# Performance work log

Measured on AMD Instinct MI355X. Metric: run time of the kernel, lower is better.

The kernel has to match this reference:

```python
import jax, jax.numpy as jnp
import numpy as np

FACTOR = 5


def setup_inputs() -> dict:
    key = jax.random.key(0)
    k1, k2, k3 = jax.random.split(key, 3)
    B, L, H, E = 8, 3072, 8, 64
    return {
        "queries": jax.random.normal(k1, (B, L, H, E), dtype=jnp.float32),
        "keys": jax.random.normal(k2, (B, L, H, E), dtype=jnp.float32),
        "values": jax.random.normal(k3, (B, L, H, E), dtype=jnp.float32),
        "attn_mask": jnp.zeros((1,), dtype=jnp.int32),  # unused, matches torch signature
    }


def _autocorrelation(queries, keys, values):
    B, L, H, E = queries.shape
    # L == S here, so keys/values are used as-is (torch path: values[:, :L])
    qp = jnp.transpose(queries, (0, 2, 3, 1))  # [B,H,E,L]
    kp = jnp.transpose(keys, (0, 2, 3, 1))     # [B,H,E,L]
    vp = jnp.transpose(values, (0, 2, 3, 1))   # [B,H,D,L]

    # period-based dependencies via FFT cross-correlation
    q_fft = jnp.fft.rfft(qp, axis=-1)
    k_fft = jnp.fft.rfft(kp, axis=-1)
    corr = jnp.fft.irfft(q_fft * jnp.conj(k_fft), n=L, axis=-1)  # [B,H,E,L]

    # time-delay aggregation (training branch of the torch module)
    top_k = int(FACTOR * np.log(L))  # static (L known at trace time)
    mean_value = corr.mean(axis=1).mean(axis=1)            # [B,L]
    weights, index = jax.lax.top_k(mean_value, top_k)      # [B,K]
    tmp_corr = jax.nn.softmax(weights, axis=-1)            # [B,K]

    # torch uses only batch-0 shifts: roll(v, -index[0,i]) == gather (t + s) mod L
    shifts = index[0]                                      # [K]
    gather_idx = (jnp.arange(L)[None, :] + shifts[:, None]) % L  # [K,L]

    def step(acc, lag):
        idx_k, w_k = lag                    # idx_k: [L], w_k: [B]
        pattern = vp[..., idx_k]            # [B,H,D,L] rolled gather
        return acc + pattern * w_k[:, None, None, None], None

    agg, _ = jax.lax.scan(step, jnp.zeros_like(vp), (gather_idx, tmp_corr.T))
    return jnp.transpose(agg, (0, 3, 1, 2))  # [B,L,H,D]


def reference(queries, keys, values, attn_mask):
    return _autocorrelation(queries, keys, values)
```

## Files before the change

kernel.cpp:

```cpp
#include <hip/hip_runtime.h>
#include <math.h>

#define L_LEN  3072
#define CH512  512
#define TOPK   40
#define NBATCH 8
#define TWSZ   1088
#define SW(i)  ((i) + ((i) >> 5))
#define FFTSZ  3168

__device__ __forceinline__ void fft3072(float* re, float* im,
                                        const float* Ctab, const float* Stab,
                                        int tid, float sgn)
{
    #pragma unroll
    for (int s = 0; s < 10; s += 2) {
        int q = 1 << s;
        #pragma unroll
        for (int ii = 0; ii < 3; ii++) {
            int ib  = tid + (ii << 8);
            int sub = ib >> 8;
            int t   = ib & 255;
            int pos = t & (q - 1);
            int base= t >> s;
            int i0  = (sub << 10) + (base << (s + 2)) + pos;
            int p0 = SW(i0), p1 = SW(i0 + q), p2 = SW(i0 + 2*q), p3 = SW(i0 + 3*q);
            int j2 = 3 * (pos << (8 - s));
            int ph = j2 + (j2 >> 4);
            float c2 = Ctab[ph], s2 = sgn * Stab[ph];
            float c1 = c2*c2 - s2*s2, s1 = 2.0f*c2*s2;
            float a0r = re[p0], a0i = im[p0];
            float a1r = re[p1], a1i = im[p1];
            float a2r = re[p2], a2i = im[p2];
            float a3r = re[p3], a3i = im[p3];
            float t1r = c1*a1r - s1*a1i, t1i = c1*a1i + s1*a1r;
            float u0r = a0r + t1r, u0i = a0i + t1i;
            float u1r = a0r - t1r, u1i = a0i - t1i;
            float t3r = c1*a3r - s1*a3i, t3i = c1*a3i + s1*a3r;
            float u2r = a2r + t3r, u2i = a2i + t3i;
            float u3r = a2r - t3r, u3i = a2i - t3i;
            float w2r = c2*u2r - s2*u2i, w2i = c2*u2i + s2*u2r;
            float w3r = c2*u3r - s2*u3i, w3i = c2*u3i + s2*u3r;
            float iw3r = -sgn * w3i, iw3i = sgn * w3r;
            re[p0] = u0r + w2r;  im[p0] = u0i + w2i;
            re[p2] = u0r - w2r;  im[p2] = u0i - w2i;
            re[p1] = u1r + iw3r; im[p1] = u1i + iw3i;
            re[p3] = u1r - iw3r; im[p3] = u1i - iw3i;
        }
        __syncthreads();
    }
    #pragma unroll
    for (int ii = 0; ii < 4; ii++) {
        int kk = tid + (ii << 8);
        int ph = kk + (kk >> 4);
        float c1 = Ctab[ph];
        float s1 = sgn * Stab[ph];
        float c2 = c1*c1 - s1*s1;
        float s2 = 2.0f*c1*s1;
        int pk0 = SW(kk), pk1 = SW(1024 + kk), pk2 = SW(2048 + kk);
        float y0r = re[pk0], y0i = im[pk0];
        float y1r = re[pk1], y1i = im[pk1];
        float y2r = re[pk2], y2i = im[pk2];
        float t1r = c1*y1r - s1*y1i, t1i = c1*y1i + s1*y1r;
        float t2r = c2*y2r - s2*y2i, t2i = c2*y2i + s2*y2r;
        float ur = t1r + t2r, ui = t1i + t2i;
        float vr = t1r - t2r, vi = t1i - t2i;
        float mr = y0r - 0.5f*ur, mi = y0i - 0.5f*ui;
        float s3 = sgn * 0.86602540378443864676f;
        re[pk0] = y0r + ur;      im[pk0] = y0i + ui;
        re[pk1] = mr - s3*vi;    im[pk1] = mi + s3*vr;
        re[pk2] = mr + s3*vi;    im[pk2] = mi - s3*vr;
    }
    __syncthreads();
}

__device__ __forceinline__ void fill_twiddles(float* Ctab, float* Stab, int tid)
{
    const float TWO_PI = 6.28318530717958647692f;
    for (int j = tid; j < 1024; j += 256) {
        float ang = TWO_PI * (float)j / 3072.0f;
        float c, s;
        __sincosf(ang, &s, &c);
        int ph = j + (j >> 4);
        Ctab[ph] = c; Stab[ph] = s;
    }
}

__global__ __launch_bounds__(256) void transpose_kernel(
    const float* __restrict__ q, const float* __restrict__ k,
    float* __restrict__ qT, float* __restrict__ kT)
{
    __shared__ float tile[64][65];
    int which = blockIdx.z & 1;
    int b     = blockIdx.z >> 1;
    int l0    = blockIdx.x << 6;
    int c0    = blockIdx.y << 6;
    int x4 = threadIdx.x & 15;
    int y  = threadIdx.x >> 4;
    const float* src = which ? k : q;
    float* dst       = which ? kT : qT;
    size_t in_base = (size_t)b * L_LEN * CH512;
    #pragma unroll
    for (int p = 0; p < 4; p++) {
        int r = y + (p << 4);
        float4 v = *(const float4*)(src + in_base + (size_t)(l0 + r) * CH512 + c0 + (x4 << 2));
        tile[r][(x4 << 2) + 0] = v.x;
        tile[r][(x4 << 2) + 1] = v.y;
        tile[r][(x4 << 2) + 2] = v.z;
        tile[r][(x4 << 2) + 3] = v.w;
    }
    __syncthreads();
    size_t out_base = (size_t)b * CH512 * L_LEN;
    #pragma unroll
    for (int p = 0; p < 4; p++) {
        int c = y + (p << 4);
        float4 w;
        w.x = tile[(x4 << 2) + 0][c];
        w.y = tile[(x4 << 2) + 1][c];
        w.z = tile[(x4 << 2) + 2][c];
        w.w = tile[(x4 << 2) + 3][c];
        *(float4*)(dst + out_base + (size_t)(c0 + c) * L_LEN + l0 + (x4 << 2)) = w;
    }
}

__global__ __launch_bounds__(256, 4) void corr_fft_kernel(
    const float* __restrict__ qT, const float* __restrict__ kT,
    float* __restrict__ S_re, float* __restrict__ S_im)
{
    __shared__ float re[FFTSZ], im[FFTSZ];
    __shared__ float Ctab[TWSZ], Stab[TWSZ];
    int blk = blockIdx.x;
    int b   = blk >> 7;
    int c0  = (blk & 127) << 2;
    int tid = threadIdx.x;

    fill_twiddles(Ctab, Stab, tid);

    float accR[12], accI[12];
    #pragma unroll
    for (int it = 0; it < 12; it++) { accR[it] = 0.0f; accI[it] = 0.0f; }

    for (int ec = 0; ec < 4; ec++) {
        size_t ch_off = ((size_t)b * CH512 + c0 + ec) * L_LEN;
        const float4* q4 = (const float4*)(qT + ch_off);
        const float4* k4 = (const float4*)(kT + ch_off);
        __syncthreads();
        #pragma unroll
        for (int it = 0; it < 3; it++) {
            int idx = tid + (it << 8);
            float4 xq = q4[idx];
            float4 xk = k4[idx];
            #pragma unroll
            for (int j = 0; j < 4; j++) {
                int n = (idx << 2) + j;
                int m = n / 3;
                int r = n - 3 * m;
                int dst = SW((r << 10) + (__brev((unsigned)m) >> 22));
                float qv = (j == 0) ? xq.x : (j == 1) ? xq.y : (j == 2) ? xq.z : xq.w;
                float kv = (j == 0) ? xk.x : (j == 1) ? xk.y : (j == 2) ? xk.z : xk.w;
                re[dst] = qv;
                im[dst] = kv;
            }
        }
        __syncthreads();
        fft3072(re, im, Ctab, Stab, tid, -1.0f);
        #pragma unroll
        for (int it = 0; it < 12; it++) {
            int f = tid + (it << 8);
            int g = (f == 0) ? 0 : (L_LEN - f);
            int pf = SW(f), pg = SW(g);
            float ar = re[pf], ai = im[pf];
            float br = re[pg], bi = -im[pg];
            float ur = ar + br, ui = ai + bi;
            float vr = ar - br, vi = ai - bi;
            accR[it] += 0.25f * (ur * vi - ui * vr);
            accI[it] += 0.25f * (ur * vr + ui * vi);
        }
    }
    #pragma unroll
    for (int it = 0; it < 12; it++) {
        int f = tid + (it << 8);
        atomicAdd(&S_re[b * L_LEN + f], accR[it]);
        atomicAdd(&S_im[b * L_LEN + f], accI[it]);
    }
}

__global__ __launch_bounds__(256) void ifft_topk_kernel(
    const float* __restrict__ S_re, const float* __restrict__ S_im,
    float* __restrict__ wts, int* __restrict__ shifts)
{
    __shared__ float re[FFTSZ], im[FFTSZ];
    __shared__ float Ctab[TWSZ], Stab[TWSZ];
    __shared__ unsigned hist[256];
    __shared__ unsigned long long s_pref;
    __shared__ unsigned s_need;
    __shared__ unsigned s_cnt;
    __shared__ unsigned selk[TOPK];
    __shared__ unsigned selidx[TOPK];
    __shared__ float sv[TOPK];
    __shared__ int   si[TOPK];

    int b = blockIdx.x;
    int tid = threadIdx.x;
    fill_twiddles(Ctab, Stab, tid);
    #pragma unroll
    for (int it = 0; it < 12; it++) {
        int n = tid + (it << 8);
        int m = n / 3;
        int r = n - 3 * m;
        int dst = SW((r << 10) + (__brev((unsigned)m) >> 22));
        re[dst] = S_re[b * L_LEN + n];
        im[dst] = S_im[b * L_LEN + n];
    }
    __syncthreads();
    fft3072(re, im, Ctab, Stab, tid, 1.0f);

    unsigned* key = (unsigned*)im;
    const float scale = 1.0f / (3072.0f * 512.0f);
    #pragma unroll
    for (int it = 0; it < 12; it++) {
        int t = tid + (it << 8);
        float v = re[SW(t)] * scale;
        unsigned u = __float_as_uint(v);
        key[t] = (u & 0x80000000u) ? ~u : (u | 0x80000000u);
    }
    if (tid == 0) { s_pref = 0ULL; s_need = TOPK; s_cnt = 0u; }
    __syncthreads();

    #pragma unroll
    for (int p = 5; p >= 0; --p) {
        hist[tid] = 0u;
        __syncthreads();
        unsigned long long pref = s_pref;
        unsigned need = s_need;
        #pragma unroll
        for (int it = 0; it < 12; it++) {
            int t = tid + (it << 8);
            unsigned long long c = ((unsigned long long)key[t] << 12) | (unsigned)(4095 - t);
            if ((c >> ((p + 1) * 8)) == (pref >> ((p + 1) * 8)))
                atomicAdd(&hist[(unsigned)((c >> (p * 8)) & 0xFFu)], 1u);
        }
        __syncthreads();
        if (tid < 64) {
            int l = tid;
            unsigned s0 = hist[4*l] + hist[4*l+1] + hist[4*l+2] + hist[4*l+3];
            unsigned T = s0;
            #pragma unroll
            for (int off = 1; off < 64; off <<= 1) {
                unsigned o = __shfl_down(T, off);
                if (l + off < 64) T += o;
            }
            unsigned above = T - s0;
            if (T >= need && above < need) {
                unsigned acc = above;
                int bin = -1;
                #pragma unroll
                for (int j = 3; j >= 0; --j) {
                    unsigned h = hist[4*l + j];
                    if (bin < 0) {
                        if (acc + h >= need) bin = 4*l + j;
                        else acc += h;
                    }
                }
                s_pref = pref | ((unsigned long long)(unsigned)bin << (p * 8));
                s_need = need - acc;
            }
        }
        __syncthreads();
    }

    unsigned long long cstar = s_pref;
    #pragma unroll
    for (int it = 0; it < 12; it++) {
        int t = tid + (it << 8);
        unsigned long long c = ((unsigned long long)key[t] << 12) | (unsigned)(4095 - t);
        if (c >= cstar) {
            unsigned pos = atomicAdd(&s_cnt, 1u);
            if (pos < TOPK) { selk[pos] = key[t]; selidx[pos] = (unsigned)t; }
        }
    }
    __syncthreads();

    if (tid < TOPK) {
        unsigned mk = selk[tid], mi = selidx[tid];
        unsigned long long mc = ((unsigned long long)mk << 12) | (unsigned)(4095 - mi);
        int rank = 0;
        #pragma unroll
        for (int j = 0; j < TOPK; j++) {
            unsigned long long cj = ((unsigned long long)selk[j] << 12) | (unsigned)(4095 - selidx[j]);
            rank += (cj > mc) ? 1 : 0;
        }
        unsigned u = (mk & 0x80000000u) ? (mk ^ 0x80000000u) : ~mk;
        sv[rank] = __uint_as_float(u);
        si[rank] = (int)mi;
    }
    __syncthreads();

    if (tid == 0) {
        float mx = sv[0];
        float sum = 0.0f;
        float ex[TOPK];
        for (int kk = 0; kk < TOPK; kk++) { ex[kk] = __expf(sv[kk] - mx); sum += ex[kk]; }
        float inv = 1.0f / sum;
        for (int kk = 0; kk < TOPK; kk++) wts[b * TOPK + kk] = ex[kk] * inv;
        if (b == 0)
            for (int kk = 0; kk < TOPK; kk++) shifts[kk] = si[kk];
    }
}

__global__ __launch_bounds__(512) void agg_kernel(
    const float* __restrict__ v, const float* __restrict__ wts,
    const int* __restrict__ shifts, float* __restrict__ out)
{
    __shared__ float4 vcol[L_LEN];
    __shared__ float w[TOPK];
    __shared__ int   sh[TOPK];
    int pid = blockIdx.x;
    int idx = ((pid & 7) << 7) + (pid >> 3);
    int cg  = idx & 127;
    int b   = idx >> 7;
    int tid = threadIdx.x;
    int ch  = cg << 2;
    if (tid < TOPK) { w[tid] = wts[b * TOPK + tid]; sh[tid] = shifts[tid]; }
    size_t vbase = (size_t)b * L_LEN * CH512 + ch;
    #pragma unroll
    for (int it = 0; it < 6; it++) {
        int r = tid + (it << 9);
        vcol[r] = *(const float4*)(v + vbase + (size_t)r * CH512);
    }
    __syncthreads();
    float4 acc0 = make_float4(0.f,0.f,0.f,0.f);
    float4 acc1 = acc0, acc2 = acc0, acc3 = acc0, acc4 = acc0, acc5 = acc0;
    #pragma unroll 8
    for (int kk = 0; kk < TOPK; kk++) {
        float ww = w[kk];
        int s = sh[kk];
        int t0 = tid + s;            if (t0 >= L_LEN) t0 -= L_LEN;
        int t1 = tid + 512 + s;      if (t1 >= L_LEN) t1 -= L_LEN;
        int t2 = tid + 1024 + s;     if (t2 >= L_LEN) t2 -= L_LEN;
        int t3 = tid + 1536 + s;     if (t3 >= L_LEN) t3 -= L_LEN;
        int t4 = tid + 2048 + s;     if (t4 >= L_LEN) t4 -= L_LEN;
        int t5 = tid + 2560 + s;     if (t5 >= L_LEN) t5 -= L_LEN;
        float4 x0 = vcol[t0], x1 = vcol[t1], x2 = vcol[t2];
        float4 x3 = vcol[t3], x4 = vcol[t4], x5 = vcol[t5];
        acc0.x += x0.x*ww; acc0.y += x0.y*ww; acc0.z += x0.z*ww; acc0.w += x0.w*ww;
        acc1.x += x1.x*ww; acc1.y += x1.y*ww; acc1.z += x1.z*ww; acc1.w += x1.w*ww;
        acc2.x += x2.x*ww; acc2.y += x2.y*ww; acc2.z += x2.z*ww; acc2.w += x2.w*ww;
        acc3.x += x3.x*ww; acc3.y += x3.y*ww; acc3.z += x3.z*ww; acc3.w += x3.w*ww;
        acc4.x += x4.x*ww; acc4.y += x4.y*ww; acc4.z += x4.z*ww; acc4.w += x4.w*ww;
        acc5.x += x5.x*ww; acc5.y += x5.y*ww; acc5.z += x5.z*ww; acc5.w += x5.w*ww;
    }
    *(float4*)(out + vbase + (size_t)(tid         ) * CH512) = acc0;
    *(float4*)(out + vbase + (size_t)(tid + 512   ) * CH512) = acc1;
    *(float4*)(out + vbase + (size_t)(tid + 1024  ) * CH512) = acc2;
    *(float4*)(out + vbase + (size_t)(tid + 1536  ) * CH512) = acc3;
    *(float4*)(out + vbase + (size_t)(tid + 2048  ) * CH512) = acc4;
    *(float4*)(out + vbase + (size_t)(tid + 2560  ) * CH512) = acc5;
}

extern "C" void kernel_launch(void* const* d_in, const int* in_sizes, int n_in,
                              void* d_out, int out_size, void* d_ws, size_t ws_size,
                              hipStream_t stream)
{
    const float* q = (const float*)d_in[0];
    const float* k = (const float*)d_in[1];
    const float* v = (const float*)d_in[2];
    float* out = (float*)d_out;
    float* ws  = (float*)d_ws;

    const size_t TSZ = (size_t)NBATCH * CH512 * L_LEN;

    float* qT = out;
    float* kT = ws;
    float* S_re = ws + TSZ;
    float* S_im = S_re + NBATCH * L_LEN;
    float* wts  = S_im + NBATCH * L_LEN;
    int*   shifts = (int*)(wts + NBATCH * TOPK);

    hipMemsetAsync(S_re, 0, (size_t)2 * NBATCH * L_LEN * sizeof(float), stream);

    transpose_kernel<<<dim3(L_LEN / 64, CH512 / 64, NBATCH * 2), dim3(256), 0, stream>>>(
        q, k, qT, kT);
    corr_fft_kernel<<<dim3(1024), dim3(256), 0, stream>>>(qT, kT, S_re, S_im);
    ifft_topk_kernel<<<dim3(NBATCH), dim3(256), 0, stream>>>(S_re, S_im, wts, shifts);
    agg_kernel<<<dim3(NBATCH * (CH512 / 4)), dim3(512), 0, stream>>>(v, wts, shifts, out);
}
```

Baseline: 312.3 us.

## Process two channels per FFT pass using packed float2 shared arrays

The correlation FFT kernel now handles two channels at once. Each shared-memory element becomes a float2 pair, and a new packed FFT routine runs its butterflies on 2-wide vectors, so the four channels per block take two FFT passes instead of four. This halves the barriers and twiddle loads per channel and can use packed FP32 math. In exchange, LDS per block roughly doubles and the launch-bounds occupancy hint drops from 4 to 2 blocks, which may reduce latency hiding.

```diff
diff --git a/kernel.cpp b/kernel.cpp
--- a/kernel.cpp
+++ b/kernel.cpp
@@ -8,6 +8,10 @@
 #define TWSZ   1088
 #define SW(i)  ((i) + ((i) >> 5))
 #define FFTSZ  3168
+#define SW2(i) ((i) + ((i) >> 4))
+#define FFTSZ2 3264
+
+typedef __attribute__((ext_vector_type(2))) float f32x2;
 
 __device__ __forceinline__ void fft3072(float* re, float* im,
                                         const float* Ctab, const float* Stab,
@@ -74,6 +78,71 @@
     __syncthreads();
 }
 
+__device__ __forceinline__ void fft3072p(f32x2* re, f32x2* im,
+                                         const float* Ctab, const float* Stab,
+                                         int tid, float sgn)
+{
+    #pragma unroll
+    for (int s = 0; s < 10; s += 2) {
+        int q = 1 << s;
+        #pragma unroll
+        for (int ii = 0; ii < 3; ii++) {
+            int ib  = tid + (ii << 8);
+            int sub = ib >> 8;
+            int t   = ib & 255;
+            int pos = t & (q - 1);
+            int base= t >> s;
+            int i0  = (sub << 10) + (base << (s + 2)) + pos;
+            int p0 = SW2(i0), p1 = SW2(i0 + q), p2 = SW2(i0 + 2*q), p3 = SW2(i0 + 3*q);
+            int j2 = 3 * (pos << (8 - s));
+            int ph = j2 + (j2 >> 4);
+            float c2 = Ctab[ph], s2 = sgn * Stab[ph];
+            float c1 = c2*c2 - s2*s2, s1 = 2.0f*c2*s2;
+            f32x2 a0r = re[p0], a0i = im[p0];
+            f32x2 a1r = re[p1], a1i = im[p1];
+            f32x2 a2r = re[p2], a2i = im[p2];
+            f32x2 a3r = re[p3], a3i = im[p3];
+            f32x2 t1r = c1*a1r - s1*a1i, t1i = c1*a1i + s1*a1r;
+            f32x2 u0r = a0r + t1r, u0i = a0i + t1i;
+            f32x2 u1r = a0r - t1r, u1i = a0i - t1i;
+            f32x2 t3r = c1*a3r - s1*a3i, t3i = c1*a3i + s1*a3r;
+            f32x2 u2r = a2r + t3r, u2i = a2i + t3i;
+            f32x2 u3r = a2r - t3r, u3i = a2i - t3i;
+            f32x2 w2r = c2*u2r - s2*u2i, w2i = c2*u2i + s2*u2r;
+            f32x2 w3r = c2*u3r - s2*u3i, w3i = c2*u3i + s2*u3r;
+            f32x2 iw3r = (-sgn) * w3i, iw3i = sgn * w3r;
+            re[p0] = u0r + w2r;  im[p0] = u0i + w2i;
+            re[p2] = u0r - w2r;  im[p2] = u0i - w2i;
+            re[p1] = u1r + iw3r; im[p1] = u1i + iw3i;
+            re[p3] = u1r - iw3r; im[p3] = u1i - iw3i;
+        }
+        __syncthreads();
+    }
+    #pragma unroll
+    for (int ii = 0; ii < 4; ii++) {
+        int kk = tid + (ii << 8);
+        int ph = kk + (kk >> 4);
+        float c1 = Ctab[ph];
+        float s1 = sgn * Stab[ph];
+        float c2 = c1*c1 - s1*s1;
+        float s2 = 2.0f*c1*s1;
+        int pk0 = SW2(kk), pk1 = SW2(1024 + kk), pk2 = SW2(2048 + kk);
+        f32x2 y0r = re[pk0], y0i = im[pk0];
+        f32x2 y1r = re[pk1], y1i = im[pk1];
+        f32x2 y2r = re[pk2], y2i = im[pk2];
+        f32x2 t1r = c1*y1r - s1*y1i, t1i = c1*y1i + s1*y1r;
+        f32x2 t2r = c2*y2r - s2*y2i, t2i = c2*y2i + s2*y2r;
+        f32x2 ur = t1r + t2r, ui = t1i + t2i;
+        f32x2 vr = t1r - t2r, vi = t1i - t2i;
+        f32x2 mr = y0r - 0.5f*ur, mi = y0i - 0.5f*ui;
+        float s3 = sgn * 0.86602540378443864676f;
+        re[pk0] = y0r + ur;      im[pk0] = y0i + ui;
+        re[pk1] = mr - s3*vi;    im[pk1] = mi + s3*vr;
+        re[pk2] = mr + s3*vi;    im[pk2] = mi - s3*vr;
+    }
+    __syncthreads();
+}
+
 __device__ __forceinline__ void fill_twiddles(float* Ctab, float* Stab, int tid)
 {
     const float TWO_PI = 6.28318530717958647692f;
@@ -123,11 +192,11 @@
     }
 }
 
-__global__ __launch_bounds__(256, 4) void corr_fft_kernel(
+__global__ __launch_bounds__(256, 2) void corr_fft_kernel(
     const float* __restrict__ qT, const float* __restrict__ kT,
     float* __restrict__ S_re, float* __restrict__ S_im)
 {
-    __shared__ float re[FFTSZ], im[FFTSZ];
+    __shared__ f32x2 re2[FFTSZ2], im2[FFTSZ2];
     __shared__ float Ctab[TWSZ], Stab[TWSZ];
     int blk = blockIdx.x;
     int b   = blk >> 7;
@@ -140,41 +209,49 @@
     #pragma unroll
     for (int it = 0; it < 12; it++) { accR[it] = 0.0f; accI[it] = 0.0f; }
 
-    for (int ec = 0; ec < 4; ec++) {
-        size_t ch_off = ((size_t)b * CH512 + c0 + ec) * L_LEN;
-        const float4* q4 = (const float4*)(qT + ch_off);
-        const float4* k4 = (const float4*)(kT + ch_off);
+    for (int pp = 0; pp < 2; pp++) {
+        int ca = c0 + (pp << 1);
+        const float4* qa4 = (const float4*)(qT + ((size_t)b * CH512 + ca) * L_LEN);
+        const float4* qb4 = (const float4*)(qT + ((size_t)b * CH512 + ca + 1) * L_LEN);
+        const float4* ka4 = (const float4*)(kT + ((size_t)b * CH512 + ca) * L_LEN);
+        const float4* kb4 = (const float4*)(kT + ((size_t)b * CH512 + ca + 1) * L_LEN);
         __syncthreads();
         #pragma unroll
         for (int it = 0; it < 3; it++) {
             int idx = tid + (it << 8);
-            float4 xq = q4[idx];
-            float4 xk = k4[idx];
+            float4 xqa = qa4[idx], xqb = qb4[idx];
+            float4 xka = ka4[idx], xkb = kb4[idx];
             #pragma unroll
             for (int j = 0; j < 4; j++) {
                 int n = (idx << 2) + j;
                 int m = n / 3;
                 int r = n - 3 * m;
-                int dst = SW((r << 10) + (__brev((unsigned)m) >> 22));
-                float qv = (j == 0) ? xq.x : (j == 1) ? xq.y : (j == 2) ? xq.z : xq.w;
-                float kv = (j == 0) ? xk.x : (j == 1) ? xk.y : (j == 2) ? xk.z : xk.w;
-                re[dst] = qv;
-                im[dst] = kv;
+                int dst = SW2((r << 10) + (__brev((unsigned)m) >> 22));
+                float qav = (j == 0) ? xqa.x : (j == 1) ? xqa.y : (j == 2) ? xqa.z : xqa.w;
+                float qbv = (j == 0) ? xqb.x : (j == 1) ? xqb.y : (j == 2) ? xqb.z : xqb.w;
+                float kav = (j == 0) ? xka.x : (j == 1) ? xka.y : (j == 2) ? xka.z : xka.w;
+                float kbv = (j == 0) ? xkb.x : (j == 1) ? xkb.y : (j == 2) ? xkb.z : xkb.w;
+                f32x2 vr = {qav, qbv};
+                f32x2 vi = {kav, kbv};
+                re2[dst] = vr;
+                im2[dst] = vi;
             }
         }
         __syncthreads();
-        fft3072(re, im, Ctab, Stab, tid, -1.0f);
+        fft3072p(re2, im2, Ctab, Stab, tid, -1.0f);
         #pragma unroll
         for (int it = 0; it < 12; it++) {
             int f = tid + (it << 8);
             int g = (f == 0) ? 0 : (L_LEN - f);
-            int pf = SW(f), pg = SW(g);
-            float ar = re[pf], ai = im[pf];
-            float br = re[pg], bi = -im[pg];
-            float ur = ar + br, ui = ai + bi;
-            float vr = ar - br, vi = ai - bi;
-            accR[it] += 0.25f * (ur * vi - ui * vr);
-            accI[it] += 0.25f * (ur * vr + ui * vi);
+            int pf = SW2(f), pg = SW2(g);
+            f32x2 ar = re2[pf], ai = im2[pf];
+            f32x2 br = re2[pg], bi = -im2[pg];
+            f32x2 ur = ar + br, ui = ai + bi;
+            f32x2 vr = ar - br, vi = ai - bi;
+            f32x2 pr = 0.25f * (ur * vi - ui * vr);
+            f32x2 pi = 0.25f * (ur * vr + ui * vi);
+            accR[it] += pr[0] + pr[1];
+            accI[it] += pi[0] + pi[1];
         }
     }
     #pragma unroll
```

Result: faster. 294.5 us (-5.7%).
